# Optimization experiments

Hardware: AMD Instinct MI355X
Metric: run time of the kernel (lower is better)

## Reference

```python
import jax, jax.numpy as jnp
import numpy as np
from jax import lax

IN_DIM, HID_DIM, OUT_DIM = 1024, 2048, 1024
N_EXP_A, TOPK_A, N_EXP_G = 12, 4, 6
BATCH = 2048
# Shannon entropy (nats) of {1/2, 1/3, 1/6}
H_TARGET = float(-(0.5 * np.log(0.5) + (1.0 / 3.0) * np.log(1.0 / 3.0) + (1.0 / 6.0) * np.log(1.0 / 6.0)))


def setup_inputs() -> dict:
    key = jax.random.key(0)
    ks = jax.random.split(key, 24)
    s_in = 1.0 / np.sqrt(IN_DIM)
    s_hid = 1.0 / np.sqrt(HID_DIM)
    s_out = 1.0 / np.sqrt(OUT_DIM)
    d = {}
    d['x'] = jax.random.normal(ks[0], (BATCH, IN_DIM), dtype=jnp.float32)
    # EngineA: gate + 12 experts (stacked)
    d['gate_a_w'] = jax.random.normal(ks[1], (IN_DIM, N_EXP_A), jnp.float32) * s_in
    d['gate_a_b'] = jnp.zeros((N_EXP_A,), jnp.float32)
    d['wa1'] = jax.random.normal(ks[2], (N_EXP_A, IN_DIM, HID_DIM), jnp.float32) * s_in
    d['ba1'] = jnp.zeros((N_EXP_A, HID_DIM), jnp.float32)
    d['wa2'] = jax.random.normal(ks[3], (N_EXP_A, HID_DIM, OUT_DIM), jnp.float32) * s_hid
    d['ba2'] = jnp.zeros((N_EXP_A, OUT_DIM), jnp.float32)
    # EngineG: gate + 6 experts (stacked)
    d['gate_g_w'] = jax.random.normal(ks[4], (IN_DIM, N_EXP_G), jnp.float32) * s_in
    d['gate_g_b'] = jnp.zeros((N_EXP_G,), jnp.float32)
    d['wg1'] = jax.random.normal(ks[5], (N_EXP_G, IN_DIM, HID_DIM), jnp.float32) * s_in
    d['bg1'] = jnp.zeros((N_EXP_G, HID_DIM), jnp.float32)
    d['wg2'] = jax.random.normal(ks[6], (N_EXP_G, HID_DIM, OUT_DIM), jnp.float32) * s_hid
    d['bg2'] = jnp.zeros((N_EXP_G, OUT_DIM), jnp.float32)
    # self_model: Linear(3,hid) Tanh Linear(hid,out) Tanh
    d['sm_w1'] = jax.random.normal(ks[7], (3, HID_DIM), jnp.float32) * (1.0 / np.sqrt(3.0))
    d['sm_b1'] = jnp.zeros((HID_DIM,), jnp.float32)
    d['sm_w2'] = jax.random.normal(ks[8], (HID_DIM, OUT_DIM), jnp.float32) * s_hid
    d['sm_b2'] = jnp.zeros((OUT_DIM,), jnp.float32)
    # self_influence Linear(out,out)
    d['si_w'] = jax.random.normal(ks[9], (OUT_DIM, OUT_DIM), jnp.float32) * s_out
    d['si_b'] = jnp.zeros((OUT_DIM,), jnp.float32)
    # field_transform Linear(out,out) + Tanh
    d['ft_w'] = jax.random.normal(ks[10], (OUT_DIM, OUT_DIM), jnp.float32) * s_out
    d['ft_b'] = jnp.zeros((OUT_DIM,), jnp.float32)
    d['tension_scale'] = jnp.asarray(1.0 / 3.0, jnp.float32)
    d['n_steps'] = 3
    return d


def _experts(x, w1, b1, w2, b2):
    # x:[B,I], w1:[E,I,H] -> [B,E,O]  (Linear-ReLU-Linear per expert)
    h = jax.nn.relu(jnp.einsum('bi,eih->beh', x, w1) + b1[None])
    return jnp.einsum('beh,eho->beo', h, w2) + b2[None]


def reference(x, gate_a_w, gate_a_b, wa1, ba1, wa2, ba2,
              gate_g_w, gate_g_b, wg1, bg1, wg2, bg2,
              sm_w1, sm_b1, sm_w2, sm_b2, si_w, si_b, ft_w, ft_b,
              tension_scale, n_steps):
    B = x.shape[0]
    # ---- EngineA: top-k (k=4 of 12) MoE ----
    logits_a = x @ gate_a_w + gate_a_b
    topv, topi = lax.top_k(logits_a, TOPK_A)
    topw = jax.nn.softmax(topv, axis=-1)
    weights_a = jnp.zeros_like(logits_a).at[jnp.arange(B)[:, None], topi].set(topw)
    out_a = _experts(x, wa1, ba1, wa2, ba2)            # [B,12,O]
    out_plus = jnp.einsum('be,beo->bo', weights_a, out_a)
    # ---- EngineG: dense-softmax MoE + entropy loss ----
    weights_g = jax.nn.softmax(x @ gate_g_w + gate_g_b, axis=-1)
    out_g = _experts(x, wg1, bg1, wg2, bg2)            # [B,6,O]
    out_minus = jnp.einsum('be,beo->bo', weights_g, out_g)
    h_ent = -(weights_g * jnp.log(weights_g + 1e-8)).sum(-1).mean()
    entropy_loss = (h_ent - H_TARGET) ** 2
    # ---- self-referential loop ----
    repulsion = out_plus - out_minus
    prev_tension = (repulsion ** 2).sum(-1, keepdims=True)      # [B,1]
    tensions = [lax.stop_gradient(prev_tension.mean())]          # .item() detaches
    modified_repulsion = repulsion
    for step in range(n_steps):
        tension_scalar = prev_tension.mean(-1, keepdims=True)    # [B,1]
        if step == 0:
            tension_delta = jnp.zeros_like(tension_scalar)
        else:
            tension_delta = tension_scalar - tensions[-1]
        step_tensor = jnp.full_like(tension_scalar, step / n_steps)
        self_input = jnp.concatenate([tension_scalar, tension_delta, step_tensor], -1)  # [B,3]
        self_state = jnp.tanh(jnp.tanh(self_input @ sm_w1 + sm_b1) @ sm_w2 + sm_b2)
        influence = self_state @ si_w + si_b
        modified_repulsion = repulsion + influence
        prev_tension = (modified_repulsion ** 2).sum(-1, keepdims=True)
        tensions.append(lax.stop_gradient(prev_tension.mean()))
    equilibrium = (out_plus + out_minus) * 0.5
    field_direction = jnp.tanh(modified_repulsion @ ft_w + ft_b)
    output = equilibrium + tension_scale * jnp.sqrt(prev_tension + 1e-8) * field_direction
    t = jnp.stack(tensions)
    convergence_loss = jnp.abs(t[1:] - t[:-1]).mean()            # built from .item()s -> constant
    aux_loss = entropy_loss + 0.001 * convergence_loss
    return output, aux_loss
```

## Files before the change

kernel.cpp:

```cpp
#include <hip/hip_runtime.h>

typedef _Float16 f16;
typedef f16  f16x8 __attribute__((ext_vector_type(8)));
typedef f16  f16x4 __attribute__((ext_vector_type(4)));
typedef float f32x4 __attribute__((ext_vector_type(4)));

#define LOAD_LDS16(gp, lp) __builtin_amdgcn_global_load_lds( \
    (const __attribute__((address_space(1))) void*)(gp),     \
    (__attribute__((address_space(3))) void*)(lp), 16, 0, 0)


__global__ __launch_bounds__(256) void transpose_cast2(const float* __restrict__ s0,
                                                       const float* __restrict__ s1,
                                                       int zsplit, f16* __restrict__ dst,
                                                       int R, int C, long sbatch,
                                                       long dbatch, int dld) {
  __shared__ float tile[32][33];
  const int zc = blockIdx.x * 32;
  const int zr = blockIdx.y * 32;
  const int z  = blockIdx.z;
  const float* s = (z < zsplit) ? (s0 + (long)z * sbatch)
                                : (s1 + (long)(z - zsplit) * sbatch);
  f16* d = dst + (long)z * dbatch;
  const int tx = threadIdx.x & 31, ty = threadIdx.x >> 5;
#pragma unroll
  for (int rr = 0; rr < 32; rr += 8)
    tile[ty + rr][tx] = s[(long)(zr + ty + rr) * C + (zc + tx)];
  __syncthreads();
#pragma unroll
  for (int rr = 0; rr < 32; rr += 8)
    d[(long)(zc + ty + rr) * dld + (zr + tx)] = (f16)tile[tx][ty + rr];
}

struct TDesc { const float* s; f16* d; int R; int C; int dld; };
struct TDesc3 { TDesc m[3]; };

__global__ __launch_bounds__(256) void transpose3(TDesc3 p) {
  const TDesc t = p.m[blockIdx.z];
  const int zc = blockIdx.x * 32;
  const int zr = blockIdx.y * 32;
  if (zr >= t.R || zc >= t.C) return;
  __shared__ float tile[32][33];
  const int tx = threadIdx.x & 31, ty = threadIdx.x >> 5;
#pragma unroll
  for (int rr = 0; rr < 32; rr += 8)
    tile[ty + rr][tx] = t.s[(long)(zr + ty + rr) * t.C + (zc + tx)];
  __syncthreads();
#pragma unroll
  for (int rr = 0; rr < 32; rr += 8)
    t.d[(long)(zc + ty + rr) * t.dld + (zr + tx)] = (f16)tile[tx][ty + rr];
}

__global__ __launch_bounds__(256) void gating_kernel(
    const float* __restrict__ x, const float* __restrict__ gaw,
    const float* __restrict__ gab, const float* __restrict__ ggw,
    const float* __restrict__ ggb, f16* __restrict__ xb,
    float* __restrict__ wG, float* __restrict__ ent,
    int* __restrict__ rows, float* __restrict__ gval, int* __restrict__ cnt,
    int* __restrict__ eA, int* __restrict__ posA, float* __restrict__ wA4) {
  const int b = blockIdx.x, t = threadIdx.x;
  const float* xr = x + (long)b * 1024;
  float pa[12], pg[6];
#pragma unroll
  for (int e = 0; e < 12; e++) pa[e] = 0.f;
#pragma unroll
  for (int e = 0; e < 6; e++) pg[e] = 0.f;
  const int i0 = t * 4;
  const float4 xv = *(const float4*)(xr + i0);
  f16x4 hx; hx.x = (f16)xv.x; hx.y = (f16)xv.y; hx.z = (f16)xv.z; hx.w = (f16)xv.w;
  *(f16x4*)(xb + (long)b * 1024 + i0) = hx;
  const float xs[4] = {xv.x, xv.y, xv.z, xv.w};
#pragma unroll
  for (int u = 0; u < 4; u++) {
    const float xi = xs[u];
    const float* ga = gaw + (long)(i0 + u) * 12;
    const float* gg = ggw + (long)(i0 + u) * 6;
#pragma unroll
    for (int e = 0; e < 12; e++) pa[e] += xi * ga[e];
#pragma unroll
    for (int e = 0; e < 6; e++) pg[e] += xi * gg[e];
  }
#pragma unroll
  for (int e = 0; e < 12; e++)
    for (int m = 1; m < 64; m <<= 1) pa[e] += __shfl_xor(pa[e], m);
#pragma unroll
  for (int e = 0; e < 6; e++)
    for (int m = 1; m < 64; m <<= 1) pg[e] += __shfl_xor(pg[e], m);
  __shared__ float rw[4][18];
  const int lane = t & 63, wv = t >> 6;
  if (lane == 0) {
#pragma unroll
    for (int e = 0; e < 12; e++) rw[wv][e] = pa[e];
#pragma unroll
    for (int e = 0; e < 6; e++) rw[wv][12 + e] = pg[e];
  }
  __syncthreads();
  if (t == 0) {
    float la[12], lg[6];
#pragma unroll
    for (int e = 0; e < 12; e++)
      la[e] = rw[0][e] + rw[1][e] + rw[2][e] + rw[3][e] + gab[e];
#pragma unroll
    for (int e = 0; e < 6; e++)
      lg[e] = rw[0][12 + e] + rw[1][12 + e] + rw[2][12 + e] + rw[3][12 + e] + ggb[e];
    unsigned used = 0; float tv[4]; int tix[4];
    for (int k = 0; k < 4; k++) {
      float best = -3.4e38f; int bi = 0;
      for (int e = 0; e < 12; e++)
        if (!((used >> e) & 1u) && la[e] > best) { best = la[e]; bi = e; }
      tv[k] = best; tix[k] = bi; used |= 1u << bi;
    }
    const float mx = tv[0];
    float s = 0.f, w4[4];
    for (int k = 0; k < 4; k++) { w4[k] = expf(tv[k] - mx); s += w4[k]; }
    for (int k = 0; k < 4; k++) {
      const float w = w4[k] / s;
      const int e = tix[k];
      const int pos = atomicAdd(&cnt[e], 1);
      rows[e * 2048 + pos] = b;
      gval[e * 2048 + pos] = w;
      eA[b * 4 + k] = e;
      posA[b * 4 + k] = pos;
      wA4[b * 4 + k] = w;
    }
    float mg = lg[0];
    for (int e = 1; e < 6; e++) mg = fmaxf(mg, lg[e]);
    float sg = 0.f, wg6[6];
    for (int e = 0; e < 6; e++) { wg6[e] = expf(lg[e] - mg); sg += wg6[e]; }
    float H = 0.f;
    for (int e = 0; e < 6; e++) {
      const float w = wg6[e] / sg;
      wG[b * 6 + e] = w;
      H -= w * logf(w + 1e-8f);
    }
    ent[b] = H;
  }
}

__global__ void base_kernel(const int* __restrict__ cnt, int* __restrict__ baseA) {
  if (threadIdx.x == 0 && blockIdx.x == 0) {
    int r = 0;
    for (int e = 0; e < 12; e++) { baseA[e] = r; r += cnt[e]; }
  }
}

__global__ __launch_bounds__(256) void combine_kernel(
    const f16* __restrict__ res, const int* __restrict__ eA,
    const int* __restrict__ posA, const float* __restrict__ wA4,
    const float* __restrict__ wG, const int* __restrict__ baseA,
    const float* __restrict__ ba2, const float* __restrict__ bg2,
    float* __restrict__ outP, float* __restrict__ outM,
    float* __restrict__ pt0, float* __restrict__ ts0) {
  const long b = blockIdx.x;
  const int t = threadIdx.x;
  const int c = t * 4;
  float4 P = {0.f, 0.f, 0.f, 0.f}, M = {0.f, 0.f, 0.f, 0.f};
#pragma unroll
  for (int k = 0; k < 4; k++) {
    const int e = eA[b * 4 + k];
    const long slot = baseA[e] + posA[b * 4 + k];
    const f16x4 v = *(const f16x4*)(res + slot * 1024 + c);
    const float w = wA4[b * 4 + k];
    const float4 bb = *(const float4*)(ba2 + (long)e * 1024 + c);
    P.x += (float)v.x + w * bb.x; P.y += (float)v.y + w * bb.y;
    P.z += (float)v.z + w * bb.z; P.w += (float)v.w + w * bb.w;
  }
#pragma unroll
  for (int e = 0; e < 6; e++) {
    const f16x4 v = *(const f16x4*)(res + (8192L + e * 2048 + b) * 1024 + c);
    const float w = wG[b * 6 + e];
    const float4 bb = *(const float4*)(bg2 + (long)e * 1024 + c);
    M.x += (float)v.x + w * bb.x; M.y += (float)v.y + w * bb.y;
    M.z += (float)v.z + w * bb.z; M.w += (float)v.w + w * bb.w;
  }
  *(float4*)(outP + b * 1024 + c) = P;
  *(float4*)(outM + b * 1024 + c) = M;
  const float dx = P.x - M.x, dy = P.y - M.y, dz = P.z - M.z, dw = P.w - M.w;
  float s = dx * dx + dy * dy + dz * dz + dw * dw;
#pragma unroll
  for (int m = 1; m < 64; m <<= 1) s += __shfl_xor(s, m);
  __shared__ float rw[4];
  if ((t & 63) == 0) rw[t >> 6] = s;
  __syncthreads();
  if (t == 0) {
    const float tot = rw[0] + rw[1] + rw[2] + rw[3];
    pt0[b] = tot;
    atomicAdd(ts0, tot);
  }
}

__global__ __launch_bounds__(256) void hsm_kernel(
    const float* __restrict__ pt, const float* __restrict__ tsum,
    const float* __restrict__ w1, const float* __restrict__ b1,
    f16* __restrict__ o, int step) {
  const int j = blockIdx.x * 256 + threadIdx.x;
  const int b0 = blockIdx.y * 64;
  const float u0 = w1[j], u1 = w1[2048 + j], u2 = w1[4096 + j], bb = b1[j];
  const float tm = tsum[0] * (1.f / 2048.f);
  const float st = (float)step * (1.f / 3.f);
#pragma unroll 4
  for (int r = 0; r < 64; r++) {
    const int b = b0 + r;
    const float t = pt[b];
    const float delta = (step == 0) ? 0.f : (t - tm);
    o[(long)b * 2048 + j] = (f16)tanhf(t * u0 + delta * u1 + st * u2 + bb);
  }
}

__global__ __launch_bounds__(256) void gemm1_kernel(
    const f16* __restrict__ x, const f16* __restrict__ w1t,
    const float* __restrict__ ba1, const float* __restrict__ bg1,
    f16* __restrict__ h, const int* __restrict__ rows,
    const float* __restrict__ gval, const int* __restrict__ cnt,
    const int* __restrict__ baseA, const float* __restrict__ wG) {
  __shared__ f16 Al[2][128 * 32];
  __shared__ f16 Bl[2][128 * 32];
  __shared__ int   Lrow[128];
  __shared__ float Lg[128];
  int id = blockIdx.x;
  int e18, mi, ni, live; long row0; const float* bp;
  if (id < 3072) {
    const int k = id & 7, t = id >> 3;
    mi = t & 15; const int pid = k * 24 + (t >> 4);
    const int e = pid >> 4; ni = pid & 15;
    live = cnt[e] - mi * 128;
    if (live <= 0) return;
    if (live > 128) live = 128;
    row0 = baseA[e] + mi * 128; e18 = e; bp = ba1 + (long)e * 2048;
  } else {
    id -= 3072;
    const int k = id & 7, t = id >> 3;
    mi = t & 15; const int pid = k * 12 + (t >> 4);
    const int e = pid >> 4; ni = pid & 15;
    row0 = 8192L + e * 2048 + mi * 128; live = 128;
    e18 = 12 + e; bp = bg1 + (long)e * 2048;
  }
  const int tid = threadIdx.x;
  const bool routed = (e18 < 12);
  if (tid < 128) {
    const int gi = mi * 128 + tid;
    if (routed) {
      const bool ok = tid < live;
      Lrow[tid] = ok ? rows[e18 * 2048 + gi] : 0;
      Lg[tid]   = ok ? gval[e18 * 2048 + gi] : 0.f;
    } else {
      Lrow[tid] = gi;
      Lg[tid] = wG[gi * 6 + (e18 - 12)];
    }
  }
  __syncthreads();
  const int sc = ((tid & 3) ^ ((tid >> 3) & 3)) * 8;
  const int r0 = Lrow[tid >> 2], r1 = Lrow[64 + (tid >> 2)];
  const f16* a0 = x + (long)r0 * 1024 + sc;
  const f16* a1 = x + (long)r1 * 1024 + sc;
  const f16* b0 = w1t + (long)e18 * 2048 * 1024 + ((long)ni * 128 + (tid >> 2)) * 1024 + sc;
  const f16* b1p = b0 + 64 * 1024;

  const int wave = tid >> 6, lane = tid & 63;
  const int wm = wave & 1, wn = wave >> 1;
  const int l16 = lane & 15, q = lane >> 4;
  const int qa = (q ^ ((l16 >> 1) & 3)) * 8;
  f32x4 acc[4][4] = {};

  LOAD_LDS16(a0, &Al[0][tid * 8]);
  LOAD_LDS16(a1, &Al[0][(256 + tid) * 8]);
  LOAD_LDS16(b0, &Bl[0][tid * 8]);
  LOAD_LDS16(b1p, &Bl[0][(256 + tid) * 8]);
  for (int kk = 0; kk < 32; ++kk) {
    __syncthreads();
    const int cur = kk & 1;
    if (kk + 1 < 32) {
      const long k0 = (long)(kk + 1) * 32;
      const int nb = cur ^ 1;
      LOAD_LDS16(a0 + k0, &Al[nb][tid * 8]);
      LOAD_LDS16(a1 + k0, &Al[nb][(256 + tid) * 8]);
      LOAD_LDS16(b0 + k0, &Bl[nb][tid * 8]);
      LOAD_LDS16(b1p + k0, &Bl[nb][(256 + tid) * 8]);
    }
    f16x8 av[4], bv[4];
#pragma unroll
    for (int i = 0; i < 4; i++)
      av[i] = *(const f16x8*)&Al[cur][(wm * 64 + i * 16 + l16) * 32 + qa];
#pragma unroll
    for (int j = 0; j < 4; j++)
      bv[j] = *(const f16x8*)&Bl[cur][(wn * 64 + j * 16 + l16) * 32 + qa];
#pragma unroll
    for (int i = 0; i < 4; i++)
#pragma unroll
      for (int j = 0; j < 4; j++)
        acc[i][j] = __builtin_amdgcn_mfma_f32_16x16x32_f16(av[i], bv[j], acc[i][j], 0, 0, 0);
  }
#pragma unroll
  for (int i = 0; i < 4; i++) {
#pragma unroll
    for (int r = 0; r < 4; r++) {
      const int lr = wm * 64 + i * 16 + q * 4 + r;
      if (lr < live) {
        const float wv = Lg[lr];
        f16* C = h + (row0 + lr) * 2048;
#pragma unroll
        for (int j = 0; j < 4; j++) {
          const int gc = ni * 128 + wn * 64 + j * 16 + l16;
          const float v = fmaxf(acc[i][j][r] + bp[gc], 0.f) * wv;
          C[gc] = (f16)v;
        }
      }
    }
  }
}

__global__ __launch_bounds__(256) void gemm2_kernel(
    const f16* __restrict__ h, const f16* __restrict__ w2t,
    f16* __restrict__ res, const int* __restrict__ cnt,
    const int* __restrict__ baseA) {
  __shared__ f16 Al[2][128 * 32];
  __shared__ f16 Bl[2][128 * 32];
  int id = blockIdx.x;
  int e18, mi, ni, live; long row0;
  if (id < 1536) {
    const int k = id & 7, t = id >> 3;
    mi = t & 15; const int pid = k * 12 + (t >> 4);
    const int e = pid >> 3; ni = pid & 7;
    live = cnt[e] - mi * 128;
    if (live <= 0) return;
    if (live > 128) live = 128;
    row0 = baseA[e] + mi * 128; e18 = e;
  } else {
    id -= 1536;
    const int k = id & 7, t = id >> 3;
    mi = t & 15; const int pid = k * 6 + (t >> 4);
    const int e = pid >> 3; ni = pid & 7;
    row0 = 8192L + e * 2048 + mi * 128; live = 128; e18 = 12 + e;
  }
  const int tid = threadIdx.x;
  const int sc = ((tid & 3) ^ ((tid >> 3) & 3)) * 8;
  const f16* a0 = h + (row0 + (tid >> 2)) * 2048 + sc;
  const f16* a1 = a0 + 64 * 2048;
  const f16* b0 = w2t + (long)e18 * 1024 * 2048 + ((long)ni * 128 + (tid >> 2)) * 2048 + sc;
  const f16* b1p = b0 + 64 * 2048;

  const int wave = tid >> 6, lane = tid & 63;
  const int wm = wave & 1, wn = wave >> 1;
  const int l16 = lane & 15, q = lane >> 4;
  const int qa = (q ^ ((l16 >> 1) & 3)) * 8;
  f32x4 acc[4][4] = {};

  LOAD_LDS16(a0, &Al[0][tid * 8]);
  LOAD_LDS16(a1, &Al[0][(256 + tid) * 8]);
  LOAD_LDS16(b0, &Bl[0][tid * 8]);
  LOAD_LDS16(b1p, &Bl[0][(256 + tid) * 8]);
  for (int kk = 0; kk < 64; ++kk) {
    __syncthreads();
    const int cur = kk & 1;
    if (kk + 1 < 64) {
      const long k0 = (long)(kk + 1) * 32;
      const int nb = cur ^ 1;
      LOAD_LDS16(a0 + k0, &Al[nb][tid * 8]);
      LOAD_LDS16(a1 + k0, &Al[nb][(256 + tid) * 8]);
      LOAD_LDS16(b0 + k0, &Bl[nb][tid * 8]);
      LOAD_LDS16(b1p + k0, &Bl[nb][(256 + tid) * 8]);
    }
    f16x8 av[4], bv[4];
#pragma unroll
    for (int i = 0; i < 4; i++)
      av[i] = *(const f16x8*)&Al[cur][(wm * 64 + i * 16 + l16) * 32 + qa];
#pragma unroll
    for (int j = 0; j < 4; j++)
      bv[j] = *(const f16x8*)&Bl[cur][(wn * 64 + j * 16 + l16) * 32 + qa];
#pragma unroll
    for (int i = 0; i < 4; i++)
#pragma unroll
      for (int j = 0; j < 4; j++)
        acc[i][j] = __builtin_amdgcn_mfma_f32_16x16x32_f16(av[i], bv[j], acc[i][j], 0, 0, 0);
  }
#pragma unroll
  for (int i = 0; i < 4; i++) {
#pragma unroll
    for (int r = 0; r < 4; r++) {
      const int lr = wm * 64 + i * 16 + q * 4 + r;
      if (lr < live) {
        f16* C = res + (row0 + lr) * 1024 + ni * 128;
#pragma unroll
        for (int j = 0; j < 4; j++) {
          const int gc = wn * 64 + j * 16 + l16;
          C[gc] = (f16)acc[i][j][r];
        }
      }
    }
  }
}


struct GA {
  const f16* A; long lda;
  const f16* B; long ldb;
  int nk;
  float* Cf; f16* Ch;
  const float* bias;
  const float* op; const float* om;
  const float* pt; const float* ts;
  float* pt_out; float* tsum_out;
  const float* ent; const float* tsb; float* aux_out;
};

template <int EPI>
__global__ __launch_bounds__(256) void gemm_s(GA a) {
  __shared__ f16 Al[2][64 * 64];
  __shared__ f16 Bl[2][64 * 64];
  const int tid = threadIdx.x;
  const int wave = tid >> 6, lane = tid & 63;
  const int wm = wave & 1, wn = wave >> 1;
  const int l16 = lane & 15, q = lane >> 4;
  const long m0 = (long)blockIdx.y * 64;
  const long n0 = (long)blockIdx.x * 64;
  const int srow = tid >> 3;
  const int sch  = ((tid & 7) ^ (srow & 7)) * 8;
  const f16* a0 = a.A + (m0 + srow) * a.lda + sch;
  const f16* a1 = a.A + (m0 + srow + 32) * a.lda + sch;
  const f16* b0 = a.B + (n0 + srow) * a.ldb + sch;
  const f16* b1 = a.B + (n0 + srow + 32) * a.ldb + sch;
  const int rx = (l16 & 7) * 8;
  f32x4 acc[2][2] = {};
  LOAD_LDS16(a0, &Al[0][tid * 8]);
  LOAD_LDS16(a1, &Al[0][(256 + tid) * 8]);
  LOAD_LDS16(b0, &Bl[0][tid * 8]);
  LOAD_LDS16(b1, &Bl[0][(256 + tid) * 8]);
  for (int kk = 0; kk < a.nk; ++kk) {
    __syncthreads();
    const int cur = kk & 1;
    if (kk + 1 < a.nk) {
      const long k0 = (long)(kk + 1) * 64;
      const int nb = cur ^ 1;
      LOAD_LDS16(a0 + k0, &Al[nb][tid * 8]);
      LOAD_LDS16(a1 + k0, &Al[nb][(256 + tid) * 8]);
      LOAD_LDS16(b0 + k0, &Bl[nb][tid * 8]);
      LOAD_LDS16(b1 + k0, &Bl[nb][(256 + tid) * 8]);
    }
    f16x8 av[2][2], bv[2][2];
#pragma unroll
    for (int hf = 0; hf < 2; hf++) {
      const int cA = (((hf * 4 + q) * 8) ^ rx);
#pragma unroll
      for (int i = 0; i < 2; i++)
        av[hf][i] = *(const f16x8*)&Al[cur][(wm * 32 + i * 16 + l16) * 64 + cA];
#pragma unroll
      for (int j = 0; j < 2; j++)
        bv[hf][j] = *(const f16x8*)&Bl[cur][(wn * 32 + j * 16 + l16) * 64 + cA];
    }
#pragma unroll
    for (int hf = 0; hf < 2; hf++)
#pragma unroll
      for (int i = 0; i < 2; i++)
#pragma unroll
        for (int j = 0; j < 2; j++)
          acc[i][j] = __builtin_amdgcn_mfma_f32_16x16x32_f16(av[hf][i], bv[hf][j], acc[i][j], 0, 0, 0);
  }
  if constexpr (EPI == 2) {
#pragma unroll
    for (int i = 0; i < 2; i++)
#pragma unroll
      for (int r = 0; r < 4; r++) {
        const long gr = m0 + wm * 32 + i * 16 + q * 4 + r;
#pragma unroll
        for (int j = 0; j < 2; j++) {
          const int gc = (int)n0 + wn * 32 + j * 16 + l16;
          a.Ch[gr * 1024 + gc] = (f16)tanhf(acc[i][j][r] + a.bias[gc]);
        }
      }
  } else if constexpr (EPI == 3) {
    float wave_ss = 0.f;
#pragma unroll
    for (int i = 0; i < 2; i++)
#pragma unroll
      for (int r = 0; r < 4; r++) {
        const long gr = m0 + wm * 32 + i * 16 + q * 4 + r;
        float ss = 0.f;
#pragma unroll
        for (int j = 0; j < 2; j++) {
          const int gc = (int)n0 + wn * 32 + j * 16 + l16;
          const long ix = gr * 1024 + gc;
          const float v = (a.op[ix] - a.om[ix]) + acc[i][j][r] + a.bias[gc];
          a.Ch[ix] = (f16)v;
          ss += v * v;
        }
        ss += __shfl_xor(ss, 1); ss += __shfl_xor(ss, 2);
        ss += __shfl_xor(ss, 4); ss += __shfl_xor(ss, 8);
        if (l16 == 0) {
          atomicAdd(a.pt_out + gr, ss);
          wave_ss += ss;
        }
      }
    wave_ss += __shfl_xor(wave_ss, 16);
    wave_ss += __shfl_xor(wave_ss, 32);
    if (lane == 0) atomicAdd(a.tsum_out, wave_ss);
  } else {
    const float tsc = a.ts[0];
#pragma unroll
    for (int i = 0; i < 2; i++)
#pragma unroll
      for (int r = 0; r < 4; r++) {
        const long gr = m0 + wm * 32 + i * 16 + q * 4 + r;
        const float sq = sqrtf(a.pt[gr] + 1e-8f) * tsc;
#pragma unroll
        for (int j = 0; j < 2; j++) {
          const int gc = (int)n0 + wn * 32 + j * 16 + l16;
          const long ix = gr * 1024 + gc;
          const float v = tanhf(acc[i][j][r] + a.bias[gc]);
          a.Cf[ix] = 0.5f * (a.op[ix] + a.om[ix]) + sq * v;
        }
      }
    if (blockIdx.x == 0 && blockIdx.y == 0) {
      float s = 0.f;
      for (int i = tid; i < 2048; i += 256) s += a.ent[i];
#pragma unroll
      for (int m = 1; m < 64; m <<= 1) s += __shfl_xor(s, m);
      __shared__ float rwa[4];
      if ((tid & 63) == 0) rwa[tid >> 6] = s;
      __syncthreads();
      if (tid == 0) {
        const float hh = (rwa[0] + rwa[1] + rwa[2] + rwa[3]) * (1.f / 2048.f);
        const float dd = hh - 1.0114042647f;
        const float el = dd * dd;
        const float t0 = a.tsb[0] * (1.f / 2048.f), t1 = a.tsb[1] * (1.f / 2048.f);
        const float t2 = a.tsb[2] * (1.f / 2048.f), t3 = a.tsb[3] * (1.f / 2048.f);
        const float conv = (fabsf(t1 - t0) + fabsf(t2 - t1) + fabsf(t3 - t2)) * (1.f / 3.f);
        a.aux_out[0] = el + 0.001f * conv;
      }
    }
  }
}


extern "C" void kernel_launch(void* const* d_in, const int* in_sizes, int n_in,
                              void* d_out, int out_size, void* d_ws, size_t ws_size,
                              hipStream_t stream) {
  (void)in_sizes; (void)n_in; (void)out_size; (void)ws_size;
  const float* x    = (const float*)d_in[0];
  const float* gaw  = (const float*)d_in[1];
  const float* gab  = (const float*)d_in[2];
  const float* wa1  = (const float*)d_in[3];
  const float* ba1  = (const float*)d_in[4];
  const float* wa2  = (const float*)d_in[5];
  const float* ba2  = (const float*)d_in[6];
  const float* ggw  = (const float*)d_in[7];
  const float* ggb  = (const float*)d_in[8];
  const float* wg1  = (const float*)d_in[9];
  const float* bg1  = (const float*)d_in[10];
  const float* wg2  = (const float*)d_in[11];
  const float* bg2  = (const float*)d_in[12];
  const float* smw1 = (const float*)d_in[13];
  const float* smb1 = (const float*)d_in[14];
  const float* smw2 = (const float*)d_in[15];
  const float* smb2 = (const float*)d_in[16];
  const float* siw  = (const float*)d_in[17];
  const float* sib  = (const float*)d_in[18];
  const float* ftw  = (const float*)d_in[19];
  const float* ftb  = (const float*)d_in[20];
  const float* tsc  = (const float*)d_in[21];

  char* p = (char*)d_ws;
  size_t off = 0;
  auto alloc = [&](size_t bytes) -> char* {
    char* r = p + off;
    off = (off + bytes + 255) & ~(size_t)255;
    return r;
  };
  f16* xb     = (f16*)alloc(2048UL * 1024 * 2);
  f16* w1t    = (f16*)alloc(18UL * 2048 * 1024 * 2);
  f16* smw2t  = (f16*)alloc(1024UL * 2048 * 2);
  f16* sit    = (f16*)alloc(1024UL * 1024 * 2);
  f16* ftt    = (f16*)alloc(1024UL * 1024 * 2);
  f16* h      = (f16*)alloc(20480UL * 2048 * 2);
  f16* res    = (f16*)alloc(20480UL * 1024 * 2);
  float* outP = (float*)alloc(2048UL * 1024 * 4);
  float* outM = (float*)alloc(2048UL * 1024 * 4);
  f16* hsmb   = (f16*)alloc(2048UL * 2048 * 2);
  f16* sst    = (f16*)alloc(2048UL * 1024 * 2);
  f16* modb   = (f16*)alloc(2048UL * 1024 * 2);
  float* entb = (float*)alloc(2048 * 4);
  float* wGb  = (float*)alloc(2048 * 6 * 4);
  float* ptb  = (float*)alloc(4 * 2048 * 4);
  float* tsb  = (float*)alloc(4 * 4);
  int*   cntb = (int*)alloc(12 * 4);
  int*   baseAb = (int*)alloc(12 * 4);
  int*   rowsb  = (int*)alloc(12 * 2048 * 4);
  float* gvalb  = (float*)alloc(12 * 2048 * 4);
  int*   eAb    = (int*)alloc(2048 * 4 * 4);
  int*   posAb  = (int*)alloc(2048 * 4 * 4);
  float* wA4b   = (float*)alloc(2048 * 4 * 4);

  f16* w2t = w1t;

  hipMemsetAsync(ptb, 0, 33072, stream);

  transpose_cast2<<<dim3(64, 32, 18), 256, 0, stream>>>(wa1, wg1, 12, w1t,
      1024, 2048, 1024L * 2048, 2048L * 1024, 1024);
  {
    TDesc3 td;
    td.m[0] = {smw2, smw2t, 2048, 1024, 2048};
    td.m[1] = {siw,  sit,  1024, 1024, 1024};
    td.m[2] = {ftw,  ftt,  1024, 1024, 1024};
    transpose3<<<dim3(32, 64, 3), 256, 0, stream>>>(td);
  }
  gating_kernel<<<2048, 256, 0, stream>>>(x, gaw, gab, ggw, ggb, xb, wGb, entb,
                                          rowsb, gvalb, cntb, eAb, posAb, wA4b);
  base_kernel<<<1, 64, 0, stream>>>(cntb, baseAb);

  gemm1_kernel<<<4608, 256, 0, stream>>>(xb, w1t, ba1, bg1, h,
                                         rowsb, gvalb, cntb, baseAb, wGb);

  transpose_cast2<<<dim3(32, 64, 18), 256, 0, stream>>>(wa2, wg2, 12, w2t,
      2048, 1024, 2048L * 1024, 1024L * 2048, 2048);

  gemm2_kernel<<<2304, 256, 0, stream>>>(h, w2t, res, cntb, baseAb);

  combine_kernel<<<2048, 256, 0, stream>>>(res, eAb, posAb, wA4b, wGb, baseAb,
                                           ba2, bg2, outP, outM, ptb, tsb);

  for (int s = 0; s < 3; s++) {
    hsm_kernel<<<dim3(8, 32), 256, 0, stream>>>(ptb + s * 2048, tsb + s, smw1, smb1, hsmb, s);
    GA g3{};
    g3.A = hsmb; g3.lda = 2048; g3.B = smw2t; g3.ldb = 2048; g3.nk = 32;
    g3.Ch = sst; g3.bias = smb2;
    gemm_s<2><<<dim3(16, 32), 256, 0, stream>>>(g3);
    GA g4{};
    g4.A = sst; g4.lda = 1024; g4.B = sit; g4.ldb = 1024; g4.nk = 16;
    g4.Ch = modb; g4.bias = sib; g4.op = outP; g4.om = outM;
    g4.pt_out = ptb + (s + 1) * 2048; g4.tsum_out = tsb + (s + 1);
    gemm_s<3><<<dim3(16, 32), 256, 0, stream>>>(g4);
  }

  GA g5{};
  g5.A = modb; g5.lda = 1024; g5.B = ftt; g5.ldb = 1024; g5.nk = 16;
  g5.Cf = (float*)d_out; g5.bias = ftb; g5.op = outP; g5.om = outM;
  g5.pt = ptb + 3 * 2048; g5.ts = tsc;
  g5.ent = entb; g5.tsb = tsb; g5.aux_out = (float*)d_out + 2048UL * 1024;
  gemm_s<4><<<dim3(16, 32), 256, 0, stream>>>(g5);
}
```

Before: 1.016 ms.

## Enlarge MoE GEMM tiles to 256x256 with 8-wave ping-pong pipelined schedule

Both expert GEMMs move from 128x128 tiles with 4 waves to 256x256 tiles with 8 waves (512 threads). The K loop becomes a hand-scheduled pipeline: LDS is split into half-K buffers, global-to-LDS loads are interleaved with MFMA clusters, and explicit barriers, waitcnt, sched_barrier and setprio calls control overlap. The goal is to raise arithmetic intensity per byte loaded and hide load latency behind MFMA work. The costs are many more accumulator registers, 64KB of LDS per block, fewer blocks for load balancing across routed experts, and a fragile manual schedule.

```diff
diff --git a/kernel.cpp b/kernel.cpp
--- a/kernel.cpp
+++ b/kernel.cpp
@@ -8,6 +8,61 @@
 #define LOAD_LDS16(gp, lp) __builtin_amdgcn_global_load_lds( \
     (const __attribute__((address_space(1))) void*)(gp),     \
     (__attribute__((address_space(3))) void*)(lp), 16, 0, 0)
+
+#define BARX() __builtin_amdgcn_s_barrier()
+#define SB0() __builtin_amdgcn_sched_barrier(0)
+#define WLG0() asm volatile("s_waitcnt lgkmcnt(0)" ::: "memory")
+#define WVM8() asm volatile("s_waitcnt vmcnt(8)" ::: "memory")
+#define WVM0() asm volatile("s_waitcnt vmcnt(0)" ::: "memory")
+
+#define ST_A(TT, BB, KH) { \
+  const long ko_ = (long)((TT) < NKC ? (TT) : (NKC - 1)) * 64 + (KH) * 32; \
+  LOAD_LDS16(pa0 + ko_, &Al[BB][KH][tid * 8]); \
+  LOAD_LDS16(pa1 + ko_, &Al[BB][KH][(512 + tid) * 8]); }
+#define ST_B(TT, BB, KH) { \
+  const long ko_ = (long)((TT) < NKC ? (TT) : (NKC - 1)) * 64 + (KH) * 32; \
+  LOAD_LDS16(pb0 + ko_, &Bl[BB][KH][tid * 8]); \
+  LOAD_LDS16(pb1 + ko_, &Bl[BB][KH][(512 + tid) * 8]); }
+
+#define RD_AV(BB, KH) _Pragma("unroll") \
+  for (int i_ = 0; i_ < 8; i_++) \
+    av[i_] = *(const f16x8*)&Al[BB][KH][(arow + i_ * 16) * 32 + qa];
+#define RD_BV(BB, KH, CB) _Pragma("unroll") \
+  for (int j_ = 0; j_ < 2; j_++) \
+    bv[j_] = *(const f16x8*)&Bl[BB][KH][(brow + (CB) * 32 + j_ * 16) * 32 + qa];
+#define MF16(CB) \
+  __builtin_amdgcn_s_setprio(1); \
+  _Pragma("unroll") \
+  for (int i_ = 0; i_ < 8; i_++) { \
+    acc[i_][2 * (CB)]     = __builtin_amdgcn_mfma_f32_16x16x32_f16(av[i_], bv[0], acc[i_][2 * (CB)], 0, 0, 0); \
+    acc[i_][2 * (CB) + 1] = __builtin_amdgcn_mfma_f32_16x16x32_f16(av[i_], bv[1], acc[i_][2 * (CB) + 1], 0, 0, 0); \
+  } \
+  __builtin_amdgcn_s_setprio(0);
+
+#define GTILE(KT, BUF) { \
+  RD_AV(BUF, 0) RD_BV(BUF, 0, 0) \
+  ST_A((KT) + 1, (BUF) ^ 1, 1) \
+  BARX(); WLG0(); SB0(); \
+  MF16(0) \
+  SB0(); BARX(); \
+  RD_BV(BUF, 0, 1) \
+  ST_B((KT) + 1, (BUF) ^ 1, 1) \
+  WVM8(); \
+  BARX(); WLG0(); SB0(); \
+  MF16(1) \
+  SB0(); BARX(); \
+  RD_AV(BUF, 1) RD_BV(BUF, 1, 0) \
+  ST_A((KT) + 2, (BUF), 0) \
+  BARX(); WLG0(); SB0(); \
+  MF16(0) \
+  SB0(); BARX(); \
+  RD_BV(BUF, 1, 1) \
+  ST_B((KT) + 2, (BUF), 0) \
+  WVM8(); \
+  BARX(); WLG0(); SB0(); \
+  MF16(1) \
+  SB0(); BARX(); \
+}
 
 
 __global__ __launch_bounds__(256) void transpose_cast2(const float* __restrict__ s0,
@@ -207,38 +262,39 @@
   }
 }
 
-__global__ __launch_bounds__(256) void gemm1_kernel(
+__global__ __launch_bounds__(512, 2) void gemm1_kernel(
     const f16* __restrict__ x, const f16* __restrict__ w1t,
     const float* __restrict__ ba1, const float* __restrict__ bg1,
     f16* __restrict__ h, const int* __restrict__ rows,
     const float* __restrict__ gval, const int* __restrict__ cnt,
     const int* __restrict__ baseA, const float* __restrict__ wG) {
-  __shared__ f16 Al[2][128 * 32];
-  __shared__ f16 Bl[2][128 * 32];
-  __shared__ int   Lrow[128];
-  __shared__ float Lg[128];
+  constexpr int NKC = 16;
+  __shared__ f16 Al[2][2][8192];
+  __shared__ f16 Bl[2][2][8192];
+  __shared__ int   Lrow[256];
+  __shared__ float Lg[256];
   int id = blockIdx.x;
   int e18, mi, ni, live; long row0; const float* bp;
-  if (id < 3072) {
+  if (id < 768) {
     const int k = id & 7, t = id >> 3;
-    mi = t & 15; const int pid = k * 24 + (t >> 4);
-    const int e = pid >> 4; ni = pid & 15;
-    live = cnt[e] - mi * 128;
+    mi = t & 7; const int pid = k * 12 + (t >> 3);
+    const int e = pid >> 3; ni = pid & 7;
+    live = cnt[e] - mi * 256;
     if (live <= 0) return;
-    if (live > 128) live = 128;
-    row0 = baseA[e] + mi * 128; e18 = e; bp = ba1 + (long)e * 2048;
+    if (live > 256) live = 256;
+    row0 = baseA[e] + mi * 256; e18 = e; bp = ba1 + (long)e * 2048;
   } else {
-    id -= 3072;
+    id -= 768;
     const int k = id & 7, t = id >> 3;
-    mi = t & 15; const int pid = k * 12 + (t >> 4);
-    const int e = pid >> 4; ni = pid & 15;
-    row0 = 8192L + e * 2048 + mi * 128; live = 128;
+    mi = t & 7; const int pid = k * 6 + (t >> 3);
+    const int e = pid >> 3; ni = pid & 7;
+    row0 = 8192L + e * 2048 + mi * 256; live = 256;
     e18 = 12 + e; bp = bg1 + (long)e * 2048;
   }
   const int tid = threadIdx.x;
   const bool routed = (e18 < 12);
-  if (tid < 128) {
-    const int gi = mi * 128 + tid;
+  if (tid < 256) {
+    const int gi = mi * 256 + tid;
     if (routed) {
       const bool ok = tid < live;
       Lrow[tid] = ok ? rows[e18 * 2048 + gi] : 0;
@@ -249,142 +305,97 @@
     }
   }
   __syncthreads();
-  const int sc = ((tid & 3) ^ ((tid >> 3) & 3)) * 8;
-  const int r0 = Lrow[tid >> 2], r1 = Lrow[64 + (tid >> 2)];
-  const f16* a0 = x + (long)r0 * 1024 + sc;
-  const f16* a1 = x + (long)r1 * 1024 + sc;
-  const f16* b0 = w1t + (long)e18 * 2048 * 1024 + ((long)ni * 128 + (tid >> 2)) * 1024 + sc;
-  const f16* b1p = b0 + 64 * 1024;
-
+  const int srow = tid >> 2;
+  const int sch = ((tid & 3) ^ ((tid >> 3) & 3)) * 8;
+  const f16* pa0 = x + (long)Lrow[srow] * 1024 + sch;
+  const f16* pa1 = x + (long)Lrow[128 + srow] * 1024 + sch;
+  const f16* pb0 = w1t + (long)e18 * 2048 * 1024 + ((long)ni * 256 + srow) * 1024 + sch;
+  const f16* pb1 = pb0 + 128 * 1024;
   const int wave = tid >> 6, lane = tid & 63;
   const int wm = wave & 1, wn = wave >> 1;
   const int l16 = lane & 15, q = lane >> 4;
   const int qa = (q ^ ((l16 >> 1) & 3)) * 8;
-  f32x4 acc[4][4] = {};
-
-  LOAD_LDS16(a0, &Al[0][tid * 8]);
-  LOAD_LDS16(a1, &Al[0][(256 + tid) * 8]);
-  LOAD_LDS16(b0, &Bl[0][tid * 8]);
-  LOAD_LDS16(b1p, &Bl[0][(256 + tid) * 8]);
-  for (int kk = 0; kk < 32; ++kk) {
-    __syncthreads();
-    const int cur = kk & 1;
-    if (kk + 1 < 32) {
-      const long k0 = (long)(kk + 1) * 32;
-      const int nb = cur ^ 1;
-      LOAD_LDS16(a0 + k0, &Al[nb][tid * 8]);
-      LOAD_LDS16(a1 + k0, &Al[nb][(256 + tid) * 8]);
-      LOAD_LDS16(b0 + k0, &Bl[nb][tid * 8]);
-      LOAD_LDS16(b1p + k0, &Bl[nb][(256 + tid) * 8]);
-    }
-    f16x8 av[4], bv[4];
-#pragma unroll
-    for (int i = 0; i < 4; i++)
-      av[i] = *(const f16x8*)&Al[cur][(wm * 64 + i * 16 + l16) * 32 + qa];
-#pragma unroll
-    for (int j = 0; j < 4; j++)
-      bv[j] = *(const f16x8*)&Bl[cur][(wn * 64 + j * 16 + l16) * 32 + qa];
-#pragma unroll
-    for (int i = 0; i < 4; i++)
-#pragma unroll
-      for (int j = 0; j < 4; j++)
-        acc[i][j] = __builtin_amdgcn_mfma_f32_16x16x32_f16(av[i], bv[j], acc[i][j], 0, 0, 0);
-  }
-#pragma unroll
-  for (int i = 0; i < 4; i++) {
+  const int arow = wm * 128 + l16;
+  const int brow = wn * 64 + l16;
+  f32x4 acc[8][4] = {};
+  f16x8 av[8], bv[2];
+  ST_A(0, 0, 0) ST_B(0, 0, 0) ST_A(0, 0, 1) ST_B(0, 0, 1) ST_A(1, 1, 0) ST_B(1, 1, 0)
+  WVM8(); BARX(); SB0();
+#pragma unroll 1
+  for (int kt = 0; kt < NKC; kt += 2) { GTILE(kt, 0) GTILE(kt + 1, 1) }
+  WVM0();
+#pragma unroll
+  for (int i = 0; i < 8; i++) {
 #pragma unroll
     for (int r = 0; r < 4; r++) {
-      const int lr = wm * 64 + i * 16 + q * 4 + r;
+      const int lr = wm * 128 + i * 16 + q * 4 + r;
       if (lr < live) {
         const float wv = Lg[lr];
-        f16* C = h + (row0 + lr) * 2048;
-#pragma unroll
-        for (int j = 0; j < 4; j++) {
-          const int gc = ni * 128 + wn * 64 + j * 16 + l16;
-          const float v = fmaxf(acc[i][j][r] + bp[gc], 0.f) * wv;
-          C[gc] = (f16)v;
+        f16* C = h + (row0 + lr) * 2048 + ni * 256;
+#pragma unroll
+        for (int jj = 0; jj < 4; jj++) {
+          const int cc = wn * 64 + jj * 16 + l16;
+          const float v = fmaxf(acc[i][jj][r] + bp[ni * 256 + cc], 0.f) * wv;
+          C[cc] = (f16)v;
         }
       }
     }
   }
 }
 
-__global__ __launch_bounds__(256) void gemm2_kernel(
+__global__ __launch_bounds__(512, 2) void gemm2_kernel(
     const f16* __restrict__ h, const f16* __restrict__ w2t,
     f16* __restrict__ res, const int* __restrict__ cnt,
     const int* __restrict__ baseA) {
-  __shared__ f16 Al[2][128 * 32];
-  __shared__ f16 Bl[2][128 * 32];
+  constexpr int NKC = 32;
+  __shared__ f16 Al[2][2][8192];
+  __shared__ f16 Bl[2][2][8192];
   int id = blockIdx.x;
   int e18, mi, ni, live; long row0;
-  if (id < 1536) {
+  if (id < 384) {
     const int k = id & 7, t = id >> 3;
-    mi = t & 15; const int pid = k * 12 + (t >> 4);
-    const int e = pid >> 3; ni = pid & 7;
-    live = cnt[e] - mi * 128;
+    mi = t & 7; const int pid = k * 6 + (t >> 3);
+    const int e = pid >> 2; ni = pid & 3;
+    live = cnt[e] - mi * 256;
     if (live <= 0) return;
-    if (live > 128) live = 128;
-    row0 = baseA[e] + mi * 128; e18 = e;
+    if (live > 256) live = 256;
+    row0 = baseA[e] + mi * 256; e18 = e;
   } else {
-    id -= 1536;
+    id -= 384;
     const int k = id & 7, t = id >> 3;
-    mi = t & 15; const int pid = k * 6 + (t >> 4);
-    const int e = pid >> 3; ni = pid & 7;
-    row0 = 8192L + e * 2048 + mi * 128; live = 128; e18 = 12 + e;
+    mi = t & 7; const int pid = k * 3 + (t >> 3);
+    const int e = pid >> 2; ni = pid & 3;
+    row0 = 8192L + e * 2048 + mi * 256; live = 256; e18 = 12 + e;
   }
   const int tid = threadIdx.x;
-  const int sc = ((tid & 3) ^ ((tid >> 3) & 3)) * 8;
-  const f16* a0 = h + (row0 + (tid >> 2)) * 2048 + sc;
-  const f16* a1 = a0 + 64 * 2048;
-  const f16* b0 = w2t + (long)e18 * 1024 * 2048 + ((long)ni * 128 + (tid >> 2)) * 2048 + sc;
-  const f16* b1p = b0 + 64 * 2048;
-
+  const int srow = tid >> 2;
+  const int sch = ((tid & 3) ^ ((tid >> 3) & 3)) * 8;
+  const f16* pa0 = h + (row0 + srow) * 2048 + sch;
+  const f16* pa1 = pa0 + 128 * 2048;
+  const f16* pb0 = w2t + (long)e18 * 1024 * 2048 + ((long)ni * 256 + srow) * 2048 + sch;
+  const f16* pb1 = pb0 + 128 * 2048;
   const int wave = tid >> 6, lane = tid & 63;
   const int wm = wave & 1, wn = wave >> 1;
   const int l16 = lane & 15, q = lane >> 4;
   const int qa = (q ^ ((l16 >> 1) & 3)) * 8;
-  f32x4 acc[4][4] = {};
-
-  LOAD_LDS16(a0, &Al[0][tid * 8]);
-  LOAD_LDS16(a1, &Al[0][(256 + tid) * 8]);
-  LOAD_LDS16(b0, &Bl[0][tid * 8]);
-  LOAD_LDS16(b1p, &Bl[0][(256 + tid) * 8]);
-  for (int kk = 0; kk < 64; ++kk) {
-    __syncthreads();
-    const int cur = kk & 1;
-    if (kk + 1 < 64) {
-      const long k0 = (long)(kk + 1) * 32;
-      const int nb = cur ^ 1;
-      LOAD_LDS16(a0 + k0, &Al[nb][tid * 8]);
-      LOAD_LDS16(a1 + k0, &Al[nb][(256 + tid) * 8]);
-      LOAD_LDS16(b0 + k0, &Bl[nb][tid * 8]);
-      LOAD_LDS16(b1p + k0, &Bl[nb][(256 + tid) * 8]);
-    }
-    f16x8 av[4], bv[4];
-#pragma unroll
-    for (int i = 0; i < 4; i++)
-      av[i] = *(const f16x8*)&Al[cur][(wm * 64 + i * 16 + l16) * 32 + qa];
-#pragma unroll
-    for (int j = 0; j < 4; j++)
-      bv[j] = *(const f16x8*)&Bl[cur][(wn * 64 + j * 16 + l16) * 32 + qa];
-#pragma unroll
-    for (int i = 0; i < 4; i++)
-#pragma unroll
-      for (int j = 0; j < 4; j++)
-        acc[i][j] = __builtin_amdgcn_mfma_f32_16x16x32_f16(av[i], bv[j], acc[i][j], 0, 0, 0);
-  }
-#pragma unroll
-  for (int i = 0; i < 4; i++) {
+  const int arow = wm * 128 + l16;
+  const int brow = wn * 64 + l16;
+  f32x4 acc[8][4] = {};
+  f16x8 av[8], bv[2];
+  ST_A(0, 0, 0) ST_B(0, 0, 0) ST_A(0, 0, 1) ST_B(0, 0, 1) ST_A(1, 1, 0) ST_B(1, 1, 0)
+  WVM8(); BARX(); SB0();
+#pragma unroll 1
+  for (int kt = 0; kt < NKC; kt += 2) { GTILE(kt, 0) GTILE(kt + 1, 1) }
+  WVM0();
+#pragma unroll
+  for (int i = 0; i < 8; i++) {
 #pragma unroll
     for (int r = 0; r < 4; r++) {
-      const int lr = wm * 64 + i * 16 + q * 4 + r;
+      const int lr = wm * 128 + i * 16 + q * 4 + r;
       if (lr < live) {
-        f16* C = res + (row0 + lr) * 1024 + ni * 128;
-#pragma unroll
-        for (int j = 0; j < 4; j++) {
-          const int gc = wn * 64 + j * 16 + l16;
-          C[gc] = (f16)acc[i][j][r];
-        }
+        f16* C = res + (row0 + lr) * 1024 + ni * 256 + wn * 64 + l16;
+#pragma unroll
+        for (int jj = 0; jj < 4; jj++) C[jj * 16] = (f16)acc[i][jj][r];
       }
     }
   }
@@ -436,16 +447,16 @@
       LOAD_LDS16(b0 + k0, &Bl[nb][tid * 8]);
       LOAD_LDS16(b1 + k0, &Bl[nb][(256 + tid) * 8]);
     }
-    f16x8 av[2][2], bv[2][2];
+    f16x8 avv[2][2], bvv[2][2];
 #pragma unroll
     for (int hf = 0; hf < 2; hf++) {
       const int cA = (((hf * 4 + q) * 8) ^ rx);
 #pragma unroll
       for (int i = 0; i < 2; i++)
-        av[hf][i] = *(const f16x8*)&Al[cur][(wm * 32 + i * 16 + l16) * 64 + cA];
+        avv[hf][i] = *(const f16x8*)&Al[cur][(wm * 32 + i * 16 + l16) * 64 + cA];
 #pragma unroll
       for (int j = 0; j < 2; j++)
-        bv[hf][j] = *(const f16x8*)&Bl[cur][(wn * 32 + j * 16 + l16) * 64 + cA];
+        bvv[hf][j] = *(const f16x8*)&Bl[cur][(wn * 32 + j * 16 + l16) * 64 + cA];
     }
 #pragma unroll
     for (int hf = 0; hf < 2; hf++)
@@ -453,7 +464,7 @@
       for (int i = 0; i < 2; i++)
 #pragma unroll
         for (int j = 0; j < 2; j++)
-          acc[i][j] = __builtin_amdgcn_mfma_f32_16x16x32_f16(av[hf][i], bv[hf][j], acc[i][j], 0, 0, 0);
+          acc[i][j] = __builtin_amdgcn_mfma_f32_16x16x32_f16(avv[hf][i], bvv[hf][j], acc[i][j], 0, 0, 0);
   }
   if constexpr (EPI == 2) {
 #pragma unroll
@@ -606,13 +617,13 @@
                                           rowsb, gvalb, cntb, eAb, posAb, wA4b);
   base_kernel<<<1, 64, 0, stream>>>(cntb, baseAb);
 
-  gemm1_kernel<<<4608, 256, 0, stream>>>(xb, w1t, ba1, bg1, h,
+  gemm1_kernel<<<1152, 512, 0, stream>>>(xb, w1t, ba1, bg1, h,
                                          rowsb, gvalb, cntb, baseAb, wGb);
 
   transpose_cast2<<<dim3(32, 64, 18), 256, 0, stream>>>(wa2, wg2, 12, w2t,
       2048, 1024, 2048L * 1024, 1024L * 2048, 2048);
 
-  gemm2_kernel<<<2304, 256, 0, stream>>>(h, w2t, res, cntb, baseAb);
+  gemm2_kernel<<<576, 512, 0, stream>>>(h, w2t, res, cntb, baseAb);
 
   combine_kernel<<<2048, 256, 0, stream>>>(res, eAb, posAb, wA4b, wGb, baseAb,
                                            ba2, bg2, outP, outM, ptb, tsb);
```

Measured after the change: 999.5 us. About the same (-1.6%).
